# Kernel tuning notes

Hardware: AMD Instinct MI355X
Metric: run time of the kernel (lower is better)

## Reference

```python
import jax, jax.numpy as jnp
import numpy as np

N_NODES = 100000
N_EDGES = 800000
IN_DIM = 128
HIDDEN = 128
CLASSES = 40


def _glorot(key, shape):
    fan_in, fan_out = shape
    lim = (6.0 / (fan_in + fan_out)) ** 0.5
    return jax.random.uniform(key, shape, jnp.float32, -lim, lim)


def setup_inputs() -> dict:
    key = jax.random.key(0)
    ks = jax.random.split(key, 8)
    x = jax.random.normal(ks[0], (N_NODES, IN_DIM), jnp.float32)
    edge_index = jax.random.randint(ks[1], (2, N_EDGES), 0, N_NODES, jnp.int64)
    # SAGEConv layer 1: lin_l (neighbor, with bias), lin_r (root, no bias)
    W1_l = _glorot(ks[2], (IN_DIM, HIDDEN))
    W1_r = _glorot(ks[3], (IN_DIM, HIDDEN))
    b1 = jnp.zeros((HIDDEN,), jnp.float32)
    # SAGEConv layer 2
    W2_l = _glorot(ks[4], (HIDDEN, CLASSES))
    W2_r = _glorot(ks[5], (HIDDEN, CLASSES))
    b2 = jnp.zeros((CLASSES,), jnp.float32)
    return {"x": x, "edge_index": edge_index, "W1_l": W1_l, "W1_r": W1_r,
            "b1": b1, "W2_l": W2_l, "W2_r": W2_r, "b2": b2}


def _sage_conv(x, src, dst, W_l, W_r, b):
    # mean aggregation of source-node features into destination nodes
    msgs = x[src]                                             # [E, d] gather
    agg = jax.ops.segment_sum(msgs, dst, num_segments=N_NODES)  # [N, d]
    cnt = jax.ops.segment_sum(jnp.ones((src.shape[0],), x.dtype), dst,
                              num_segments=N_NODES)           # [N]
    mean = agg / jnp.maximum(cnt, 1.0)[:, None]
    return mean @ W_l + x @ W_r + b


def reference(x, edge_index, W1_l, W1_r, b1, W2_l, W2_r, b2):
    src, dst = edge_index[0], edge_index[1]
    h = _sage_conv(x, src, dst, W1_l, W1_r, b1)
    h = jax.nn.relu(h)
    # F.dropout in eval mode is the identity (deterministic reference)
    out = _sage_conv(h, src, dst, W2_l, W2_r, b2)
    return out
```

## Files before the change

kernel.cpp:

```cpp
#include <hip/hip_runtime.h>
#include <hip/hip_bf16.h>

#define N_NODES 100000
#define N_EDGES 800000
#define IN_DIM  128
#define HIDDEN  128
#define CLASSES 40
#define CAP     32
#define NSH     8
#define SLICES  100
#define EPB     8000
#define BIN_B   (NSH*SLICES)
#define CAST_B  12500
#define PACK_B  24
#define CUR_STRIDE 12544

typedef __attribute__((ext_vector_type(8))) short bf16x8;
typedef __attribute__((ext_vector_type(4))) float floatx4;

__device__ __forceinline__ float bf2f(unsigned short u) {
    return __uint_as_float(((unsigned int)u) << 16);
}
__device__ __forceinline__ unsigned short f2bf(float f) {
    unsigned int u = __float_as_uint(f);
    unsigned int r = 0x7fffu + ((u >> 16) & 1u);
    return (unsigned short)((u + r) >> 16);
}
__device__ __forceinline__ int curIdx(int d) { return (d & 7) * CUR_STRIDE + (d >> 3); }

__global__ void k_prep(const int* __restrict__ src, const int* __restrict__ dst,
                       int* __restrict__ cur, int* __restrict__ csr,
                       const float* __restrict__ x, unsigned short* __restrict__ A1,
                       const float* __restrict__ W1l, const float* __restrict__ W1r,
                       unsigned short* __restrict__ Bp1,
                       const float* __restrict__ W2l, const float* __restrict__ W2r,
                       unsigned short* __restrict__ Bp2) {
    int blk = blockIdx.x;
    if (blk < BIN_B) {
        int g = blk & 7;
        int slice = blk >> 3;
        const int4* s4p = reinterpret_cast<const int4*>(src) + slice * (EPB / 4);
        const int4* d4p = reinterpret_cast<const int4*>(dst) + slice * (EPB / 4);
        for (int i = threadIdx.x; i < EPB / 4; i += 256) {
            int4 d4 = d4p[i];
            int4 s4 = s4p[i];
            #pragma unroll
            for (int j = 0; j < 4; ++j) {
                int d = (&d4.x)[j];
                if ((d & 7) == g) {
                    int s = (&s4.x)[j];
                    int slot = atomicAdd(&cur[g * CUR_STRIDE + (d >> 3)], 1);
                    if (slot < CAP) csr[d * CAP + slot] = s;
                }
            }
        }
    } else if (blk < BIN_B + CAST_B) {
        int t = (blk - BIN_B) * 256 + threadIdx.x;
        int n = t >> 5, g = t & 31;
        float4 v = reinterpret_cast<const float4*>(x + (size_t)n * 128)[g];
        ushort4 u = { f2bf(v.x), f2bf(v.y), f2bf(v.z), f2bf(v.w) };
        *(ushort4*)(A1 + (size_t)n * 256 + 128 + g * 4) = u;
    } else {
        int t = (blk - BIN_B - CAST_B) * 256 + threadIdx.x;
        if (t < 4096) {
            int o = t >> 7, n = t & 127;
            const float* W = (o < 16) ? W1l : W1r;
            int k0 = (o & 15) * 8;
            union { unsigned short us[8]; uint4 v; } pk;
            #pragma unroll
            for (int j = 0; j < 8; ++j) pk.us[j] = f2bf(W[(size_t)(k0 + j) * 128 + n]);
            *(uint4*)(Bp1 + (size_t)t * 8) = pk.v;
        } else {
            int t2 = t - 4096;
            int o = t2 >> 7, n = t2 & 127;
            const float* W = (n < 64) ? W2l : W2r;
            int col = n & 63;
            int k0 = o * 8;
            union { unsigned short us[8]; uint4 v; } pk;
            #pragma unroll
            for (int j = 0; j < 8; ++j)
                pk.us[j] = (col < 40) ? f2bf(W[(size_t)(k0 + j) * 40 + col]) : (unsigned short)0;
            *(uint4*)(Bp2 + (size_t)t2 * 8) = pk.v;
        }
    }
}

__global__ void k_agg1(unsigned short* __restrict__ A1, const int* __restrict__ deg,
                       const int* __restrict__ csr) {
    int n = blockIdx.x * 4 + (threadIdx.x >> 6);
    int lane = threadIdx.x & 63;
    if (n >= N_NODES) return;
    int cnt = min(deg[curIdx(n)], CAP);
    int nl = csr[n * CAP + (lane & (CAP - 1))];
    int r = lane >> 4, c = lane & 15;
    float acc[8] = {0.f, 0.f, 0.f, 0.f, 0.f, 0.f, 0.f, 0.f};
    for (int base = 0; base < cnt; base += 16) {
        #pragma unroll
        for (int u = 0; u < 4; ++u) {
            int e = base + u * 4 + r;
            int s = __shfl(nl, min(e, cnt - 1), 64);
            bf16x8 v = {};
            if (e < cnt)
                v = *(const bf16x8*)(A1 + (size_t)s * 256 + 128 + c * 8);
            #pragma unroll
            for (int j = 0; j < 8; ++j) acc[j] += bf2f((unsigned short)v[j]);
        }
    }
    #pragma unroll
    for (int j = 0; j < 8; ++j) {
        acc[j] += __shfl_xor(acc[j], 16, 64);
        acc[j] += __shfl_xor(acc[j], 32, 64);
    }
    if (lane < 16) {
        float inv = 1.0f / fmaxf((float)cnt, 1.0f);
        union { unsigned short us[8]; bf16x8 v; } pk;
        #pragma unroll
        for (int j = 0; j < 8; ++j) pk.us[j] = f2bf(acc[j] * inv);
        *(bf16x8*)(A1 + (size_t)n * 256 + c * 8) = pk.v;
    }
}

__global__ __launch_bounds__(256)
void k_gemm(unsigned short* __restrict__ A1, const unsigned short* __restrict__ Bp1,
            const float* __restrict__ b1, const unsigned short* __restrict__ Bp2) {
    __shared__ unsigned short Hs[4][16][136];
    int wv = threadIdx.x >> 6, lane = threadIdx.x & 63;
    int q = lane >> 4, nn = lane & 15;
    int m0 = blockIdx.x * 64 + wv * 16;
    int ma = m0 + nn;
    bool mv = (ma < N_NODES);
    const unsigned short* arow = A1 + (size_t)ma * 256;

    floatx4 acc[8] = {};
    for (int kt = 0; kt < 8; ++kt) {
        bf16x8 a = {};
        if (mv) a = *(const bf16x8*)(arow + kt * 32 + q * 8);
        bf16x8 b[8];
        #pragma unroll
        for (int nt = 0; nt < 8; ++nt)
            b[nt] = *(const bf16x8*)(Bp1 + ((size_t)((kt * 4 + q) * 128 + nt * 16 + nn)) * 8);
        #pragma unroll
        for (int nt = 0; nt < 8; ++nt)
            acc[nt] = __builtin_amdgcn_mfma_f32_16x16x32_bf16(a, b[nt], acc[nt], 0, 0, 0);
    }
    #pragma unroll
    for (int nt = 0; nt < 8; ++nt) {
        int col = nt * 16 + nn;
        float bias = b1[col];
        #pragma unroll
        for (int r = 0; r < 4; ++r)
            Hs[wv][q * 4 + r][col] = f2bf(fmaxf(acc[nt][r] + bias, 0.f));
    }
    floatx4 acc2[8] = {};
    for (int kt = 0; kt < 4; ++kt) {
        bf16x8 a = *(const bf16x8*)(&Hs[wv][nn][kt * 32 + q * 8]);
        bf16x8 b[8];
        #pragma unroll
        for (int nt = 0; nt < 8; ++nt)
            b[nt] = *(const bf16x8*)(Bp2 + ((size_t)((kt * 4 + q) * 128 + nt * 16 + nn)) * 8);
        #pragma unroll
        for (int nt = 0; nt < 8; ++nt)
            acc2[nt] = __builtin_amdgcn_mfma_f32_16x16x32_bf16(a, b[nt], acc2[nt], 0, 0, 0);
    }
    #pragma unroll
    for (int nt = 0; nt < 4; ++nt) {
        int col = nt * 16 + nn;
        #pragma unroll
        for (int r = 0; r < 4; ++r) {
            int ro = m0 + q * 4 + r;
            if (ro < N_NODES)
                A1[(size_t)ro * 256 + col] = f2bf(acc2[nt][r]);
        }
    }
    #pragma unroll
    for (int nt = 4; nt < 8; ++nt) {
        int col = (nt - 4) * 16 + nn;
        #pragma unroll
        for (int r = 0; r < 4; ++r) {
            int ro = m0 + q * 4 + r;
            if (ro < N_NODES) {
                float* Rp = (float*)(A1 + (size_t)ro * 256 + 128);
                Rp[col] = acc2[nt][r];
            }
        }
    }
}

__global__ void k_agg2(const unsigned short* __restrict__ A1, const int* __restrict__ deg,
                       const int* __restrict__ csr, const float* __restrict__ b2,
                       float* __restrict__ out) {
    int n = blockIdx.x * 4 + (threadIdx.x >> 6);
    int lane = threadIdx.x & 63;
    if (n >= N_NODES) return;
    int cnt = min(deg[curIdx(n)], CAP);
    int nl = csr[n * CAP + (lane & (CAP - 1))];
    int r = lane >> 3, c = lane & 7;
    float acc[8] = {0.f, 0.f, 0.f, 0.f, 0.f, 0.f, 0.f, 0.f};
    for (int base = 0; base < cnt; base += 16) {
        #pragma unroll
        for (int u = 0; u < 2; ++u) {
            int e = base + u * 8 + r;
            int s = __shfl(nl, min(e, cnt - 1), 64);
            bf16x8 v = {};
            if (e < cnt)
                v = *(const bf16x8*)(A1 + (size_t)s * 256 + c * 8);
            #pragma unroll
            for (int j = 0; j < 8; ++j) acc[j] += bf2f((unsigned short)v[j]);
        }
    }
    #pragma unroll
    for (int j = 0; j < 8; ++j) {
        acc[j] += __shfl_xor(acc[j], 8, 64);
        acc[j] += __shfl_xor(acc[j], 16, 64);
        acc[j] += __shfl_xor(acc[j], 32, 64);
    }
    if (lane < 5) {
        float inv = 1.0f / fmaxf((float)cnt, 1.0f);
        const float* Rrow = (const float*)(A1 + (size_t)n * 256 + 128);
        float o[8];
        #pragma unroll
        for (int j = 0; j < 8; ++j)
            o[j] = acc[j] * inv + Rrow[c * 8 + j] + b2[c * 8 + j];
        float* op = out + (size_t)n * CLASSES + c * 8;
        *(float4*)(op)     = make_float4(o[0], o[1], o[2], o[3]);
        *(float4*)(op + 4) = make_float4(o[4], o[5], o[6], o[7]);
    }
}

extern "C" void kernel_launch(void* const* d_in, const int* in_sizes, int n_in,
                              void* d_out, int out_size, void* d_ws, size_t ws_size,
                              hipStream_t stream) {
    const float* x   = (const float*)d_in[0];
    const int*   ei  = (const int*)d_in[1];
    const float* W1l = (const float*)d_in[2];
    const float* W1r = (const float*)d_in[3];
    const float* b1  = (const float*)d_in[4];
    const float* W2l = (const float*)d_in[5];
    const float* W2r = (const float*)d_in[6];
    const float* b2  = (const float*)d_in[7];
    float* out = (float*)d_out;

    const int* src = ei;
    const int* dst = ei + N_EDGES;

    char* ws = (char*)d_ws;
    size_t off = 0;
    auto alloc = [&](size_t bytes) { void* p = ws + off; off += (bytes + 511) & ~(size_t)511; return p; };
    int* cur = (int*)alloc((size_t)NSH * CUR_STRIDE * 4);
    int* csr = (int*)alloc((size_t)N_NODES * CAP * 4);
    unsigned short* Bp1 = (unsigned short*)alloc((size_t)32 * 128 * 8 * 2);
    unsigned short* Bp2 = (unsigned short*)alloc((size_t)16 * 128 * 8 * 2);
    unsigned short* A1  = (unsigned short*)alloc((size_t)N_NODES * 256 * 2);

    hipMemsetAsync(cur, 0, (size_t)NSH * CUR_STRIDE * 4, stream);

    k_prep<<<BIN_B + CAST_B + PACK_B, 256, 0, stream>>>(
        src, dst, cur, csr, x, A1, W1l, W1r, Bp1, W2l, W2r, Bp2);

    k_agg1<<<(N_NODES + 3) / 4, 256, 0, stream>>>(A1, cur, csr);
    k_gemm<<<(N_NODES + 63) / 64, 256, 0, stream>>>(A1, Bp1, b1, Bp2);
    k_agg2<<<(N_NODES + 3) / 4, 256, 0, stream>>>(A1, cur, csr, b2, out);
}
```

Before: 250.2 us.

## Fuse layer-1 aggregation into GEMM kernel and pair nodes in layer-2 aggregation

The first-layer neighbor-mean aggregation now runs inside the GEMM kernel. Each wave gathers features for its 16 rows, two nodes at a time, and writes the bf16 means straight into shared memory, so the separate aggregation kernel and its global write and re-read of the mean half of A1 go away. The root-projection output moves to a separate float buffer, because other blocks are still reading the x half of A1 while this kernel runs. The layer-2 aggregation now handles two nodes per wave to keep more independent gathers in flight. The trade-off is less parallelism in the gather phase: there are only 64 nodes per block, processed serially within each wave.

```diff
diff --git a/kernel.cpp b/kernel.cpp
--- a/kernel.cpp
+++ b/kernel.cpp
@@ -85,56 +85,77 @@
     }
 }
 
-__global__ void k_agg1(unsigned short* __restrict__ A1, const int* __restrict__ deg,
-                       const int* __restrict__ csr) {
-    int n = blockIdx.x * 4 + (threadIdx.x >> 6);
-    int lane = threadIdx.x & 63;
-    if (n >= N_NODES) return;
-    int cnt = min(deg[curIdx(n)], CAP);
-    int nl = csr[n * CAP + (lane & (CAP - 1))];
-    int r = lane >> 4, c = lane & 15;
-    float acc[8] = {0.f, 0.f, 0.f, 0.f, 0.f, 0.f, 0.f, 0.f};
-    for (int base = 0; base < cnt; base += 16) {
-        #pragma unroll
-        for (int u = 0; u < 4; ++u) {
-            int e = base + u * 4 + r;
-            int s = __shfl(nl, min(e, cnt - 1), 64);
-            bf16x8 v = {};
-            if (e < cnt)
-                v = *(const bf16x8*)(A1 + (size_t)s * 256 + 128 + c * 8);
-            #pragma unroll
-            for (int j = 0; j < 8; ++j) acc[j] += bf2f((unsigned short)v[j]);
-        }
-    }
-    #pragma unroll
-    for (int j = 0; j < 8; ++j) {
-        acc[j] += __shfl_xor(acc[j], 16, 64);
-        acc[j] += __shfl_xor(acc[j], 32, 64);
-    }
-    if (lane < 16) {
-        float inv = 1.0f / fmaxf((float)cnt, 1.0f);
-        union { unsigned short us[8]; bf16x8 v; } pk;
-        #pragma unroll
-        for (int j = 0; j < 8; ++j) pk.us[j] = f2bf(acc[j] * inv);
-        *(bf16x8*)(A1 + (size_t)n * 256 + c * 8) = pk.v;
-    }
-}
-
 __global__ __launch_bounds__(256)
-void k_gemm(unsigned short* __restrict__ A1, const unsigned short* __restrict__ Bp1,
-            const float* __restrict__ b1, const unsigned short* __restrict__ Bp2) {
-    __shared__ unsigned short Hs[4][16][136];
+void k_fused(unsigned short* __restrict__ A1, float* __restrict__ Rbuf,
+             const int* __restrict__ deg, const int* __restrict__ csr,
+             const unsigned short* __restrict__ Bp1, const float* __restrict__ b1,
+             const unsigned short* __restrict__ Bp2) {
+    __shared__ unsigned short S[4][16][136];
     int wv = threadIdx.x >> 6, lane = threadIdx.x & 63;
     int q = lane >> 4, nn = lane & 15;
     int m0 = blockIdx.x * 64 + wv * 16;
+
+    for (int i = 0; i < 16; i += 2) {
+        int nA = m0 + i, nB = m0 + i + 1;
+        int aA = min(nA, N_NODES - 1), aB = min(nB, N_NODES - 1);
+        int cntA = (nA < N_NODES) ? min(deg[curIdx(aA)], CAP) : 0;
+        int cntB = (nB < N_NODES) ? min(deg[curIdx(aB)], CAP) : 0;
+        int nl = csr[(lane < 32 ? aA : aB) * CAP + (lane & 31)];
+        float accA[8] = {}, accB[8] = {};
+        int mx = max(cntA, cntB);
+        for (int b = 0; b < mx; b += 16) {
+            #pragma unroll
+            for (int u = 0; u < 4; ++u) {
+                int e = b + u * 4 + q;
+                int iA = min(e, cntA - 1) & 31;
+                int iB = min(e, cntB - 1) & 31;
+                int sA = __shfl(nl, iA, 64);
+                int sB = __shfl(nl, 32 + iB, 64);
+                bf16x8 vA = {}, vB = {};
+                if (e < cntA) vA = *(const bf16x8*)(A1 + (size_t)sA * 256 + 128 + nn * 8);
+                if (e < cntB) vB = *(const bf16x8*)(A1 + (size_t)sB * 256 + 128 + nn * 8);
+                #pragma unroll
+                for (int j = 0; j < 8; ++j) {
+                    accA[j] += bf2f((unsigned short)vA[j]);
+                    accB[j] += bf2f((unsigned short)vB[j]);
+                }
+            }
+        }
+        #pragma unroll
+        for (int j = 0; j < 8; ++j) {
+            accA[j] += __shfl_xor(accA[j], 16, 64);
+            accA[j] += __shfl_xor(accA[j], 32, 64);
+            accB[j] += __shfl_xor(accB[j], 16, 64);
+            accB[j] += __shfl_xor(accB[j], 32, 64);
+        }
+        if (lane < 16) {
+            float invA = 1.0f / fmaxf((float)cntA, 1.0f);
+            float invB = 1.0f / fmaxf((float)cntB, 1.0f);
+            union { unsigned short us[8]; bf16x8 v; } pA, pB;
+            #pragma unroll
+            for (int j = 0; j < 8; ++j) {
+                pA.us[j] = f2bf(accA[j] * invA);
+                pB.us[j] = f2bf(accB[j] * invB);
+            }
+            *(bf16x8*)(&S[wv][i][lane * 8])     = pA.v;
+            *(bf16x8*)(&S[wv][i + 1][lane * 8]) = pB.v;
+        }
+    }
+
     int ma = m0 + nn;
     bool mv = (ma < N_NODES);
     const unsigned short* arow = A1 + (size_t)ma * 256;
 
     floatx4 acc[8] = {};
+    #pragma unroll
     for (int kt = 0; kt < 8; ++kt) {
-        bf16x8 a = {};
-        if (mv) a = *(const bf16x8*)(arow + kt * 32 + q * 8);
+        bf16x8 a;
+        if (kt < 4) {
+            a = *(const bf16x8*)(&S[wv][nn][kt * 32 + q * 8]);
+        } else {
+            a = bf16x8{};
+            if (mv) a = *(const bf16x8*)(arow + kt * 32 + q * 8);
+        }
         bf16x8 b[8];
         #pragma unroll
         for (int nt = 0; nt < 8; ++nt)
@@ -149,11 +170,12 @@
         float bias = b1[col];
         #pragma unroll
         for (int r = 0; r < 4; ++r)
-            Hs[wv][q * 4 + r][col] = f2bf(fmaxf(acc[nt][r] + bias, 0.f));
+            S[wv][q * 4 + r][col] = f2bf(fmaxf(acc[nt][r] + bias, 0.f));
     }
     floatx4 acc2[8] = {};
+    #pragma unroll
     for (int kt = 0; kt < 4; ++kt) {
-        bf16x8 a = *(const bf16x8*)(&Hs[wv][nn][kt * 32 + q * 8]);
+        bf16x8 a = *(const bf16x8*)(&S[wv][nn][kt * 32 + q * 8]);
         bf16x8 b[8];
         #pragma unroll
         for (int nt = 0; nt < 8; ++nt)
@@ -178,52 +200,71 @@
         #pragma unroll
         for (int r = 0; r < 4; ++r) {
             int ro = m0 + q * 4 + r;
-            if (ro < N_NODES) {
-                float* Rp = (float*)(A1 + (size_t)ro * 256 + 128);
-                Rp[col] = acc2[nt][r];
+            if (ro < N_NODES)
+                Rbuf[(size_t)ro * 64 + col] = acc2[nt][r];
+        }
+    }
+}
+
+__global__ void k_agg2(const unsigned short* __restrict__ A1, const float* __restrict__ Rbuf,
+                       const int* __restrict__ deg, const int* __restrict__ csr,
+                       const float* __restrict__ b2, float* __restrict__ out) {
+    int pair = blockIdx.x * 4 + (threadIdx.x >> 6);
+    int nA = pair * 2, nB = nA + 1;
+    int lane = threadIdx.x & 63;
+    if (nA >= N_NODES) return;
+    int aB = min(nB, N_NODES - 1);
+    int cntA = min(deg[curIdx(nA)], CAP);
+    int cntB = (nB < N_NODES) ? min(deg[curIdx(aB)], CAP) : 0;
+    int nl = csr[(lane < 32 ? nA : aB) * CAP + (lane & 31)];
+    int r = lane >> 3, c = lane & 7;
+    float accA[8] = {}, accB[8] = {};
+    int mx = max(cntA, cntB);
+    for (int b = 0; b < mx; b += 16) {
+        #pragma unroll
+        for (int u = 0; u < 2; ++u) {
+            int e = b + u * 8 + r;
+            int sA = __shfl(nl, min(e, cntA - 1) & 31, 64);
+            int sB = __shfl(nl, 32 + (min(e, cntB - 1) & 31), 64);
+            bf16x8 vA = {}, vB = {};
+            if (e < cntA) vA = *(const bf16x8*)(A1 + (size_t)sA * 256 + c * 8);
+            if (e < cntB) vB = *(const bf16x8*)(A1 + (size_t)sB * 256 + c * 8);
+            #pragma unroll
+            for (int j = 0; j < 8; ++j) {
+                accA[j] += bf2f((unsigned short)vA[j]);
+                accB[j] += bf2f((unsigned short)vB[j]);
             }
         }
     }
-}
-
-__global__ void k_agg2(const unsigned short* __restrict__ A1, const int* __restrict__ deg,
-                       const int* __restrict__ csr, const float* __restrict__ b2,
-                       float* __restrict__ out) {
-    int n = blockIdx.x * 4 + (threadIdx.x >> 6);
-    int lane = threadIdx.x & 63;
-    if (n >= N_NODES) return;
-    int cnt = min(deg[curIdx(n)], CAP);
-    int nl = csr[n * CAP + (lane & (CAP - 1))];
-    int r = lane >> 3, c = lane & 7;
-    float acc[8] = {0.f, 0.f, 0.f, 0.f, 0.f, 0.f, 0.f, 0.f};
-    for (int base = 0; base < cnt; base += 16) {
-        #pragma unroll
-        for (int u = 0; u < 2; ++u) {
-            int e = base + u * 8 + r;
-            int s = __shfl(nl, min(e, cnt - 1), 64);
-            bf16x8 v = {};
-            if (e < cnt)
-                v = *(const bf16x8*)(A1 + (size_t)s * 256 + c * 8);
-            #pragma unroll
-            for (int j = 0; j < 8; ++j) acc[j] += bf2f((unsigned short)v[j]);
-        }
-    }
     #pragma unroll
     for (int j = 0; j < 8; ++j) {
-        acc[j] += __shfl_xor(acc[j], 8, 64);
-        acc[j] += __shfl_xor(acc[j], 16, 64);
-        acc[j] += __shfl_xor(acc[j], 32, 64);
+        accA[j] += __shfl_xor(accA[j], 8, 64);
+        accA[j] += __shfl_xor(accA[j], 16, 64);
+        accA[j] += __shfl_xor(accA[j], 32, 64);
+        accB[j] += __shfl_xor(accB[j], 8, 64);
+        accB[j] += __shfl_xor(accB[j], 16, 64);
+        accB[j] += __shfl_xor(accB[j], 32, 64);
     }
     if (lane < 5) {
-        float inv = 1.0f / fmaxf((float)cnt, 1.0f);
-        const float* Rrow = (const float*)(A1 + (size_t)n * 256 + 128);
+        float invA = 1.0f / fmaxf((float)cntA, 1.0f);
+        const float* RrowA = Rbuf + (size_t)nA * 64;
         float o[8];
         #pragma unroll
         for (int j = 0; j < 8; ++j)
-            o[j] = acc[j] * inv + Rrow[c * 8 + j] + b2[c * 8 + j];
-        float* op = out + (size_t)n * CLASSES + c * 8;
-        *(float4*)(op)     = make_float4(o[0], o[1], o[2], o[3]);
-        *(float4*)(op + 4) = make_float4(o[4], o[5], o[6], o[7]);
+            o[j] = accA[j] * invA + RrowA[c * 8 + j] + b2[c * 8 + j];
+        float* opA = out + (size_t)nA * CLASSES + c * 8;
+        *(float4*)(opA)     = make_float4(o[0], o[1], o[2], o[3]);
+        *(float4*)(opA + 4) = make_float4(o[4], o[5], o[6], o[7]);
+        if (nB < N_NODES) {
+            float invB = 1.0f / fmaxf((float)cntB, 1.0f);
+            const float* RrowB = Rbuf + (size_t)nB * 64;
+            #pragma unroll
+            for (int j = 0; j < 8; ++j)
+                o[j] = accB[j] * invB + RrowB[c * 8 + j] + b2[c * 8 + j];
+            float* opB = out + (size_t)nB * CLASSES + c * 8;
+            *(float4*)(opB)     = make_float4(o[0], o[1], o[2], o[3]);
+            *(float4*)(opB + 4) = make_float4(o[4], o[5], o[6], o[7]);
+        }
     }
 }
 
@@ -251,13 +292,13 @@
     unsigned short* Bp1 = (unsigned short*)alloc((size_t)32 * 128 * 8 * 2);
     unsigned short* Bp2 = (unsigned short*)alloc((size_t)16 * 128 * 8 * 2);
     unsigned short* A1  = (unsigned short*)alloc((size_t)N_NODES * 256 * 2);
+    float* Rbuf = (float*)alloc((size_t)N_NODES * 64 * 4);
 
     hipMemsetAsync(cur, 0, (size_t)NSH * CUR_STRIDE * 4, stream);
 
     k_prep<<<BIN_B + CAST_B + PACK_B, 256, 0, stream>>>(
         src, dst, cur, csr, x, A1, W1l, W1r, Bp1, W2l, W2r, Bp2);
 
-    k_agg1<<<(N_NODES + 3) / 4, 256, 0, stream>>>(A1, cur, csr);
-    k_gemm<<<(N_NODES + 63) / 64, 256, 0, stream>>>(A1, Bp1, b1, Bp2);
-    k_agg2<<<(N_NODES + 3) / 4, 256, 0, stream>>>(A1, cur, csr, b2, out);
-}
+    k_fused<<<(N_NODES + 63) / 64, 256, 0, stream>>>(A1, Rbuf, cur, csr, Bp1, b1, Bp2);
+    k_agg2<<<(N_NODES / 2 + 3) / 4, 256, 0, stream>>>(A1, Rbuf, cur, csr, b2, out);
+}
```

After: 281.6 us. 1.13x slower.
